# Performance work log

Measured on AMD Instinct MI355X. Metric: run time of the kernel, lower is better.

Reference implementation:

```python
import jax, jax.numpy as jnp
import numpy as np

N = 4096   # num_agents
F = 512    # feat_dim
P = 512    # phi_dim
A = 512    # aggr_dim
S = 6      # state_dim
H = 20     # MLP hidden width (hidden_layers=(20,20))


def _lstm(X, wih, whh, b):
    # torch.nn.LSTM single layer on an unbatched sequence X: [T, in] -> [T, hidden]
    pre = X @ wih + b  # [T, 4*hidden]
    Fh = whh.shape[0]
    def step(carry, p):
        h, c = carry
        g = p + h @ whh
        i, f, gg, o = jnp.split(g, 4, axis=-1)  # torch gate order: i, f, g, o
        c = jax.nn.sigmoid(f) * c + jax.nn.sigmoid(i) * jnp.tanh(gg)
        h = jax.nn.sigmoid(o) * jnp.tanh(c)
        return (h, c), h
    init = (jnp.zeros((Fh,), X.dtype), jnp.zeros((Fh,), X.dtype))
    _, hs = jax.lax.scan(step, init, pre)
    return hs


def setup_inputs():
    key = jax.random.key(0)
    ks = jax.random.split(key, 30)
    def rn(k, shape, s=0.05):
        return (jax.random.normal(k, shape) * s).astype(jnp.float32)
    x = jax.random.normal(ks[0], (N, F), dtype=jnp.float32)
    states = jax.random.normal(ks[1], (N, S), dtype=jnp.float32)
    # one comm link per agent (E == N, required by update()'s concat with x)
    src = jax.random.randint(ks[2], (N,), 0, N)
    dst = jnp.arange(N)
    inp = dict(x=x, states=states, src=src, dst=dst)
    inp["phi_w0"] = rn(ks[3], (4, F + S, H)); inp["phi_b0"] = rn(ks[4], (4, H))
    inp["phi_w1"] = rn(ks[5], (4, H, H));     inp["phi_b1"] = rn(ks[6], (4, H))
    inp["phi_w2"] = rn(ks[7], (4, H, P));     inp["phi_b2"] = rn(ks[8], (4, P))
    inp["tq_w"] = rn(ks[9], (4, P, A));  inp["tq_b"] = rn(ks[10], (4, A))
    inp["tk_w"] = rn(ks[11], (4, P, A)); inp["tk_b"] = rn(ks[12], (4, A))
    inp["tv_w"] = rn(ks[13], (4, P, A)); inp["tv_b"] = rn(ks[14], (4, A))
    inp["ts_w"] = rn(ks[15], (4, P, A)); inp["ts_b"] = rn(ks[16], (4, A))
    inp["wih0"] = rn(ks[17], (4, A + F, 4 * F)); inp["whh0"] = rn(ks[18], (4, F, 4 * F))
    inp["b0"] = rn(ks[19], (4, 4 * F))
    inp["wih1"] = rn(ks[20], (4, F, 4 * F)); inp["whh1"] = rn(ks[21], (4, F, 4 * F))
    inp["b1"] = rn(ks[22], (4, 4 * F))
    inp["cbf_w"] = rn(ks[23], (F, 1)); inp["cbf_b"] = rn(ks[24], (1,))
    return inp


def reference(x, states, src, dst, phi_w0, phi_b0, phi_w1, phi_b1, phi_w2, phi_b2,
              tq_w, tq_b, tk_w, tk_b, tv_w, tv_b, ts_w, ts_b,
              wih0, whh0, b0, wih1, whh1, b1, cbf_w, cbf_b):
    inv_sqrt_a = 1.0 / jnp.sqrt(jnp.float32(A))

    def gnn_layer(l, xin):
        # message: phi(concat(x_j, states_j - states_i))  (j = src, i = dst)
        msg = jnp.concatenate([xin[src], states[src] - states[dst]], axis=1)  # [E, F+S]
        h = jax.nn.relu(msg @ phi_w0[l] + phi_b0[l])
        h = jax.nn.relu(h @ phi_w1[l] + phi_b1[l])
        phi = h @ phi_w2[l] + phi_b2[l]  # [E, P]
        # aggregate: TransformerConv over message rows (E == N), heads=1
        q = phi @ tq_w[l] + tq_b[l]
        k = phi @ tk_w[l] + tk_b[l]
        v = phi @ tv_w[l] + tv_b[l]
        logits = jnp.sum(q[dst] * k[src], axis=-1) * inv_sqrt_a  # [E]
        m = jax.ops.segment_max(logits, dst, num_segments=N)
        e = jnp.exp(logits - m[dst])
        ssum = jax.ops.segment_sum(e, dst, num_segments=N)
        alpha = e / ssum[dst]
        aggr = jax.ops.segment_sum(alpha[:, None] * v[src], dst, num_segments=N)
        aggr = aggr + phi @ ts_w[l] + ts_b[l]  # root/skip connection
        # update: 2-layer LSTM over agents as an unbatched sequence
        gi = jnp.concatenate([aggr, xin], axis=1)  # [N, A+F]
        h0 = _lstm(gi, wih0[l], whh0[l], b0[l])
        h1 = _lstm(h0, wih1[l], whh1[l], b1[l])
        return h1

    xcur = gnn_layer(0, x)
    xcur = jax.nn.relu(xcur)
    xcur = gnn_layer(1, xcur)
    xcur = gnn_layer(2, xcur)      # feat_transformer layer 1
    xcur = jax.nn.relu(xcur)
    xcur = gnn_layer(3, xcur)      # feat_transformer layer 2
    hcbf = jax.nn.relu(xcur) @ cbf_w + cbf_b  # feat_2_CBF
    return xcur, hcbf
```

## Files before the change

kernel.cpp:

```cpp
#include <hip/hip_runtime.h>
#include <hip/hip_bf16.h>
#include <math.h>

#define NA   4096
#define FDIM 512
#define SDIM 6
#define HID  20
#define GDIM 2048
#define LWG  32

__device__ __forceinline__ float sigf(float x) { return 1.0f / (1.0f + __expf(-x)); }
__device__ __forceinline__ float tanh_fast(float x) {
    float e = __expf(2.0f * x);
    return 1.0f - 2.0f / (e + 1.0f);
}

__device__ __forceinline__ void atomicMaxF(float* addr, float v) {
    if (v >= 0.0f) atomicMax((int*)addr, __float_as_int(v));
    else           atomicMin((unsigned int*)addr, __float_as_uint(v));
}

__global__ void __launch_bounds__(256)
phi_fused(const float* __restrict__ xin, const float* __restrict__ states,
          const int* __restrict__ src, const int* __restrict__ dst,
          const float* __restrict__ w0, const float* __restrict__ b0,
          const float* __restrict__ w1, const float* __restrict__ b1,
          const float* __restrict__ w2, const float* __restrict__ b2,
          float* __restrict__ phi)
{
    int e = blockIdx.x, tid = threadIdx.x;
    __shared__ float msgv[FDIM + SDIM];
    __shared__ float red[240];
    __shared__ float hb1[HID];
    __shared__ float hb2[HID];
    int s = src[e], d = dst[e];
    for (int i = tid; i < FDIM; i += 256) msgv[i] = xin[(size_t)s * FDIM + i];
    if (tid < SDIM) msgv[FDIM + tid] = states[s * SDIM + tid] - states[d * SDIM + tid];
    __syncthreads();
    if (tid < 240) {
        int col = tid / 12, sg = tid % 12;
        int k0 = sg * 44, k1 = min(FDIM + SDIM, k0 + 44);
        float acc = 0.0f;
        for (int k = k0; k < k1; k++) acc += msgv[k] * w0[k * HID + col];
        red[tid] = acc;
    }
    __syncthreads();
    if (tid < HID) {
        float a = b0[tid];
#pragma unroll
        for (int q = 0; q < 12; q++) a += red[tid * 12 + q];
        hb1[tid] = fmaxf(a, 0.0f);
    }
    __syncthreads();
    if (tid < HID) {
        float a = b1[tid];
#pragma unroll
        for (int k = 0; k < HID; k++) a += hb1[k] * w1[k * HID + tid];
        hb2[tid] = fmaxf(a, 0.0f);
    }
    __syncthreads();
    for (int c = tid; c < FDIM; c += 256) {
        float a = b2[c];
#pragma unroll
        for (int k = 0; k < HID; k++) a += hb2[k] * w2[k * FDIM + c];
        phi[(size_t)e * FDIM + c] = a;
    }
}

struct Ptrs4 {
    const float* B[4];
    const float* bias[4];
    float* C[4];
};

__global__ void __launch_bounds__(256)
gemm128(const float* __restrict__ A1, int lda1,
        const float* __restrict__ A2, int lda2, int splitA,
        Ptrs4 p, int M, int N, int K)
{
    __shared__ float a_lds[16][132];
    __shared__ float b_lds[16][132];
    const float* __restrict__ B    = p.B[blockIdx.z];
    const float* __restrict__ bias = p.bias[blockIdx.z];
    float* __restrict__ C          = p.C[blockIdx.z];
    const int tid = threadIdx.x;
    const int m0 = blockIdx.y * 128, n0 = blockIdx.x * 128;
    const int ar = tid >> 2, ak4 = (tid & 3) * 4;
    const int br = tid >> 5, bc4 = (tid & 31) * 4;
    const int ty = tid >> 4, tx = tid & 15;
    float acc[8][8] = {};

    for (int kt = 0; kt < K; kt += 16) {
        int ak = kt + ak4;
        const float* abase;
        int acol;
        if (ak < splitA) { abase = A1; acol = ak;
            const float* r0 = abase + (size_t)(m0 + ar) * lda1 + acol;
            const float* r1 = abase + (size_t)(m0 + ar + 64) * lda1 + acol;
            float4 a0 = *(const float4*)r0;
            float4 a1 = *(const float4*)r1;
            a_lds[ak4 + 0][ar] = a0.x; a_lds[ak4 + 1][ar] = a0.y;
            a_lds[ak4 + 2][ar] = a0.z; a_lds[ak4 + 3][ar] = a0.w;
            a_lds[ak4 + 0][ar + 64] = a1.x; a_lds[ak4 + 1][ar + 64] = a1.y;
            a_lds[ak4 + 2][ar + 64] = a1.z; a_lds[ak4 + 3][ar + 64] = a1.w;
        } else {
            acol = ak - splitA;
            const float* r0 = A2 + (size_t)(m0 + ar) * lda2 + acol;
            const float* r1 = A2 + (size_t)(m0 + ar + 64) * lda2 + acol;
            float4 a0 = *(const float4*)r0;
            float4 a1 = *(const float4*)r1;
            a_lds[ak4 + 0][ar] = a0.x; a_lds[ak4 + 1][ar] = a0.y;
            a_lds[ak4 + 2][ar] = a0.z; a_lds[ak4 + 3][ar] = a0.w;
            a_lds[ak4 + 0][ar + 64] = a1.x; a_lds[ak4 + 1][ar + 64] = a1.y;
            a_lds[ak4 + 2][ar + 64] = a1.z; a_lds[ak4 + 3][ar + 64] = a1.w;
        }
        {
            float4 b0v = *(const float4*)(B + (size_t)(kt + br) * N + n0 + bc4);
            float4 b1v = *(const float4*)(B + (size_t)(kt + br + 8) * N + n0 + bc4);
            *(float4*)&b_lds[br][bc4] = b0v;
            *(float4*)&b_lds[br + 8][bc4] = b1v;
        }
        __syncthreads();
#pragma unroll
        for (int kk = 0; kk < 16; kk++) {
            float av[8], bv[8];
            *(float4*)&av[0] = *(const float4*)&a_lds[kk][ty * 4];
            *(float4*)&av[4] = *(const float4*)&a_lds[kk][64 + ty * 4];
            *(float4*)&bv[0] = *(const float4*)&b_lds[kk][tx * 4];
            *(float4*)&bv[4] = *(const float4*)&b_lds[kk][64 + tx * 4];
#pragma unroll
            for (int i = 0; i < 8; i++)
#pragma unroll
                for (int j = 0; j < 8; j++)
                    acc[i][j] += av[i] * bv[j];
        }
        __syncthreads();
    }

    float4 bb0 = *(const float4*)(bias + n0 + tx * 4);
    float4 bb1 = *(const float4*)(bias + n0 + 64 + tx * 4);
    const float bbs0[4] = { bb0.x, bb0.y, bb0.z, bb0.w };
    const float bbs1[4] = { bb1.x, bb1.y, bb1.z, bb1.w };
#pragma unroll
    for (int i = 0; i < 8; i++) {
        int row = m0 + ((i < 4) ? (ty * 4 + i) : (64 + ty * 4 + i - 4));
        float4 o0, o1;
        o0.x = acc[i][0] + bbs0[0]; o0.y = acc[i][1] + bbs0[1];
        o0.z = acc[i][2] + bbs0[2]; o0.w = acc[i][3] + bbs0[3];
        o1.x = acc[i][4] + bbs1[0]; o1.y = acc[i][5] + bbs1[1];
        o1.z = acc[i][6] + bbs1[2]; o1.w = acc[i][7] + bbs1[3];
        *(float4*)&C[(size_t)row * N + n0 + tx * 4] = o0;
        *(float4*)&C[(size_t)row * N + n0 + 64 + tx * 4] = o1;
    }
}

__global__ void att_init(float* __restrict__ m, float* __restrict__ ssum)
{
    int i = blockIdx.x * blockDim.x + threadIdx.x;
    if (i < NA) { m[i] = -INFINITY; ssum[i] = 0.0f; }
}

__global__ void att_logits(const float* __restrict__ q, const float* __restrict__ k,
                           const int* __restrict__ src, const int* __restrict__ dst,
                           float* __restrict__ logits, float* __restrict__ m)
{
    int e = blockIdx.x, tid = threadIdx.x;
    int s = src[e], d = dst[e];
    const float4* qr = (const float4*)(q + (size_t)d * FDIM);
    const float4* kr = (const float4*)(k + (size_t)s * FDIM);
    float acc = 0.0f;
    for (int i = tid; i < FDIM / 4; i += 64) {
        float4 a = qr[i], b = kr[i];
        acc += a.x * b.x + a.y * b.y + a.z * b.z + a.w * b.w;
    }
    for (int off = 32; off; off >>= 1) acc += __shfl_down(acc, off);
    if (tid == 0) {
        float v = acc * 0.04419417382415922f;
        logits[e] = v;
        atomicMaxF(&m[d], v);
    }
}

__global__ void att_expsum(const float* __restrict__ logits, const float* __restrict__ m,
                           const int* __restrict__ dst,
                           float* __restrict__ ebuf, float* __restrict__ ssum)
{
    int e = blockIdx.x * blockDim.x + threadIdx.x;
    if (e < NA) {
        float v = __expf(logits[e] - m[dst[e]]);
        ebuf[e] = v;
        atomicAdd(&ssum[dst[e]], v);
    }
}

__global__ void att_scatter(const float* __restrict__ v, const int* __restrict__ src,
                            const int* __restrict__ dst, const float* __restrict__ ebuf,
                            const float* __restrict__ ssum, float* __restrict__ aggr)
{
    int e = blockIdx.x, tid = threadIdx.x;
    int s = src[e], d = dst[e];
    float alpha = ebuf[e] / ssum[d];
    const float* vr = v + (size_t)s * FDIM;
    float* ar = aggr + (size_t)d * FDIM;
    for (int c = tid; c < FDIM; c += 256) atomicAdd(&ar[c], alpha * vr[c]);
}

__global__ void __launch_bounds__(512, 2)
lstm_pair(const float* __restrict__ pre0, const float* __restrict__ whh0,
          const float* __restrict__ wih1, const float* __restrict__ whh1,
          const float* __restrict__ b1,
          float* __restrict__ xout,
          unsigned long long* __restrict__ hfull,
          unsigned long long* __restrict__ hbuf1,
          unsigned int tag0, unsigned int tag1, int T)
{
    const int wg = blockIdx.x;
    const bool roleB = wg >= LWG;
    const int w = wg & (LWG - 1);
    const int tid = threadIdx.x;
    const int dl = tid & 15;
    const int gate = (tid >> 4) & 3;
    const int seg = tid >> 6;
    const int j = gate * 512 + w * 16 + dl;

    float wreg[128];
    if (!roleB) {
        const float* wc = whh0 + (size_t)(seg * 64) * GDIM + j;
#pragma unroll
        for (int kk = 0; kk < 64; kk++) wreg[kk] = wc[(size_t)kk * GDIM];
    } else {
        const float* wc = (seg < 4)
            ? (wih1 + (size_t)(seg * 128) * GDIM + j)
            : (whh1 + (size_t)((seg - 4) * 128) * GDIM + j);
#pragma unroll
        for (int kk = 0; kk < 128; kk++) wreg[kk] = wc[(size_t)kk * GDIM];
    }

    __shared__ float h_lds[1024];
    __shared__ float red[512];
    __shared__ float gbuf[64];
    float c = 0.0f;
    float extra = 0.0f;
    if (tid < 64) extra = roleB ? b1[j] : pre0[j];
    if (!roleB) h_lds[tid] = 0.0f;
    else        h_lds[512 + tid] = 0.0f;
    __syncthreads();

    if (!roleB) {
        for (int t = 0; t < T; t++) {
            const float* hseg = h_lds + seg * 64;
            float a0 = 0, a1 = 0, a2 = 0, a3 = 0;
#pragma unroll
            for (int kk = 0; kk < 64; kk += 4) {
                float4 hv = *(const float4*)(hseg + kk);
                a0 += wreg[kk + 0] * hv.x;
                a1 += wreg[kk + 1] * hv.y;
                a2 += wreg[kk + 2] * hv.z;
                a3 += wreg[kk + 3] * hv.w;
            }
            red[tid] = (a0 + a1) + (a2 + a3);
            __syncthreads();
            if (tid < 64) {
                float tot = extra;
#pragma unroll
                for (int s = 0; s < 8; s++) tot += red[tid + 64 * s];
                gbuf[tid] = tot;
                if (t + 1 < T) extra = pre0[(size_t)(t + 1) * GDIM + j];
            }
            __syncthreads();
            if (tid < 16) {
                float ii = gbuf[tid], ff = gbuf[16 + tid], gg = gbuf[32 + tid], oo = gbuf[48 + tid];
                c = sigf(ff) * c + sigf(ii) * tanh_fast(gg);
                float h = sigf(oo) * tanh_fast(c);
                unsigned long long word =
                    ((unsigned long long)(tag0 + (unsigned)t + 1u) << 32) |
                    (unsigned long long)__float_as_uint(h);
                __hip_atomic_store(&hfull[(size_t)t * 512 + w * 16 + tid], word,
                                   __ATOMIC_RELAXED, __HIP_MEMORY_SCOPE_AGENT);
            }
            if (t + 1 < T) {
                unsigned long long want = tag0 + (unsigned)t + 1u;
                const unsigned long long* p = &hfull[(size_t)t * 512 + tid];
                unsigned long long v = __hip_atomic_load(p, __ATOMIC_RELAXED, __HIP_MEMORY_SCOPE_AGENT);
                while ((v >> 32) != want)
                    v = __hip_atomic_load(p, __ATOMIC_RELAXED, __HIP_MEMORY_SCOPE_AGENT);
                h_lds[tid] = __uint_as_float((unsigned)v);
                __syncthreads();
            }
        }
    } else {
        for (int t = 0; t < T; t++) {
            {
                unsigned long long want = tag0 + (unsigned)t + 1u;
                const unsigned long long* p = &hfull[(size_t)t * 512 + tid];
                unsigned long long v = __hip_atomic_load(p, __ATOMIC_RELAXED, __HIP_MEMORY_SCOPE_AGENT);
                while ((v >> 32) != want)
                    v = __hip_atomic_load(p, __ATOMIC_RELAXED, __HIP_MEMORY_SCOPE_AGENT);
                h_lds[tid] = __uint_as_float((unsigned)v);
            }
            __syncthreads();
            const float* hseg = h_lds + seg * 128;
            float a0 = 0, a1 = 0, a2 = 0, a3 = 0;
#pragma unroll
            for (int kk = 0; kk < 128; kk += 4) {
                float4 hv = *(const float4*)(hseg + kk);
                a0 += wreg[kk + 0] * hv.x;
                a1 += wreg[kk + 1] * hv.y;
                a2 += wreg[kk + 2] * hv.z;
                a3 += wreg[kk + 3] * hv.w;
            }
            red[tid] = (a0 + a1) + (a2 + a3);
            __syncthreads();
            if (tid < 64) {
                float tot = extra;
#pragma unroll
                for (int s = 0; s < 8; s++) tot += red[tid + 64 * s];
                gbuf[tid] = tot;
            }
            __syncthreads();
            if (tid < 16) {
                float ii = gbuf[tid], ff = gbuf[16 + tid], gg = gbuf[32 + tid], oo = gbuf[48 + tid];
                c = sigf(ff) * c + sigf(ii) * tanh_fast(gg);
                float h = sigf(oo) * tanh_fast(c);
                xout[(size_t)t * 512 + w * 16 + tid] = h;
                unsigned long long word =
                    ((unsigned long long)(tag1 + (unsigned)t + 1u) << 32) |
                    (unsigned long long)__float_as_uint(h);
                __hip_atomic_store(&hbuf1[(t & 1) * 512 + w * 16 + tid], word,
                                   __ATOMIC_RELAXED, __HIP_MEMORY_SCOPE_AGENT);
            }
            if (t + 1 < T) {
                unsigned long long want = tag1 + (unsigned)t + 1u;
                const unsigned long long* p = &hbuf1[(t & 1) * 512 + tid];
                unsigned long long v = __hip_atomic_load(p, __ATOMIC_RELAXED, __HIP_MEMORY_SCOPE_AGENT);
                while ((v >> 32) != want)
                    v = __hip_atomic_load(p, __ATOMIC_RELAXED, __HIP_MEMORY_SCOPE_AGENT);
                h_lds[512 + tid] = __uint_as_float((unsigned)v);
                __syncthreads();
            }
        }
    }
}

__global__ void relu_ip(float* __restrict__ x, int n)
{
    int i = blockIdx.x * blockDim.x + threadIdx.x;
    if (i < n) x[i] = fmaxf(x[i], 0.0f);
}

__global__ void cbf_head(const float* __restrict__ xc, const float* __restrict__ w,
                         const float* __restrict__ b, float* __restrict__ out)
{
    int i = blockIdx.x, tid = threadIdx.x;
    const float* xr = xc + (size_t)i * FDIM;
    float acc = 0.0f;
    for (int d = tid; d < FDIM; d += 64) acc += fmaxf(xr[d], 0.0f) * w[d];
    for (int off = 32; off; off >>= 1) acc += __shfl_down(acc, off);
    if (tid == 0) out[i] = acc + b[0];
}

__global__ void zero_u64(unsigned long long* __restrict__ p, int n)
{
    int i = blockIdx.x * blockDim.x + threadIdx.x;
    int stride = gridDim.x * blockDim.x;
    for (; i < n; i += stride) p[i] = 0ull;
}

extern "C" void kernel_launch(void* const* d_in, const int* in_sizes, int n_in,
                              void* d_out, int out_size, void* d_ws, size_t ws_size,
                              hipStream_t stream)
{
    const float* x      = (const float*)d_in[0];
    const float* states = (const float*)d_in[1];
    const int*   src    = (const int*)d_in[2];
    const int*   dst    = (const int*)d_in[3];
    const float* phi_w0 = (const float*)d_in[4];
    const float* phi_b0 = (const float*)d_in[5];
    const float* phi_w1 = (const float*)d_in[6];
    const float* phi_b1 = (const float*)d_in[7];
    const float* phi_w2 = (const float*)d_in[8];
    const float* phi_b2 = (const float*)d_in[9];
    const float* tq_w = (const float*)d_in[10]; const float* tq_b = (const float*)d_in[11];
    const float* tk_w = (const float*)d_in[12]; const float* tk_b = (const float*)d_in[13];
    const float* tv_w = (const float*)d_in[14]; const float* tv_b = (const float*)d_in[15];
    const float* ts_w = (const float*)d_in[16]; const float* ts_b = (const float*)d_in[17];
    const float* wih0 = (const float*)d_in[18]; const float* whh0 = (const float*)d_in[19];
    const float* b0   = (const float*)d_in[20];
    const float* wih1 = (const float*)d_in[21]; const float* whh1 = (const float*)d_in[22];
    const float* b1   = (const float*)d_in[23];
    const float* cbf_w = (const float*)d_in[24]; const float* cbf_b = (const float*)d_in[25];

    float* ws = (float*)d_ws;
    size_t off = 0;
    auto alloc = [&](size_t n) { float* p = ws + off; off += n; return p; };
    float* xA     = alloc((size_t)NA * FDIM);
    float* xB     = alloc((size_t)NA * FDIM);
    float* phi    = alloc((size_t)NA * FDIM);
    float* qb     = alloc((size_t)NA * FDIM);
    float* kb     = alloc((size_t)NA * FDIM);
    float* vb     = alloc((size_t)NA * FDIM);
    float* aggr   = alloc((size_t)NA * FDIM);
    float* pre    = alloc((size_t)NA * GDIM);
    float* logits = alloc(NA);
    float* mb     = alloc(NA);
    float* ssum   = alloc(NA);
    float* ebuf   = alloc(NA);
    const int HFULL_WORDS = NA * 512;
    unsigned long long* hfull = (unsigned long long*)alloc((size_t)2 * (HFULL_WORDS + 1024));
    unsigned long long* hbuf1 = hfull + HFULL_WORDS;

    float* out_x   = (float*)d_out;
    float* out_cbf = out_x + (size_t)NA * FDIM;

    zero_u64<<<2048, 256, 0, stream>>>(hfull, HFULL_WORDS + 1024);

    const float* xin = x;
    for (int l = 0; l < 4; l++) {
        float* xout = (l == 3) ? out_x : ((l & 1) ? xB : xA);

        phi_fused<<<NA, 256, 0, stream>>>(xin, states, src, dst,
            phi_w0 + (size_t)l * 518 * HID, phi_b0 + l * HID,
            phi_w1 + (size_t)l * HID * HID, phi_b1 + l * HID,
            phi_w2 + (size_t)l * HID * FDIM, phi_b2 + l * FDIM, phi);

        {
            Ptrs4 p;
            p.B[0] = tq_w + (size_t)l * FDIM * FDIM; p.bias[0] = tq_b + l * FDIM; p.C[0] = qb;
            p.B[1] = tk_w + (size_t)l * FDIM * FDIM; p.bias[1] = tk_b + l * FDIM; p.C[1] = kb;
            p.B[2] = tv_w + (size_t)l * FDIM * FDIM; p.bias[2] = tv_b + l * FDIM; p.C[2] = vb;
            p.B[3] = ts_w + (size_t)l * FDIM * FDIM; p.bias[3] = ts_b + l * FDIM; p.C[3] = aggr;
            gemm128<<<dim3(FDIM / 128, NA / 128, 4), 256, 0, stream>>>(
                phi, FDIM, phi, FDIM, FDIM, p, NA, FDIM, FDIM);
        }

        att_init<<<NA / 256, 256, 0, stream>>>(mb, ssum);
        att_logits<<<NA, 64, 0, stream>>>(qb, kb, src, dst, logits, mb);
        att_expsum<<<NA / 256, 256, 0, stream>>>(logits, mb, dst, ebuf, ssum);
        att_scatter<<<NA, 256, 0, stream>>>(vb, src, dst, ebuf, ssum, aggr);

        {
            Ptrs4 p;
            p.B[0] = wih0 + (size_t)l * 1024 * GDIM; p.bias[0] = b0 + (size_t)l * GDIM; p.C[0] = pre;
            p.B[1] = p.B[0]; p.bias[1] = p.bias[0]; p.C[1] = pre;
            p.B[2] = p.B[0]; p.bias[2] = p.bias[0]; p.C[2] = pre;
            p.B[3] = p.B[0]; p.bias[3] = p.bias[0]; p.C[3] = pre;
            gemm128<<<dim3(GDIM / 128, NA / 128, 1), 256, 0, stream>>>(
                aggr, FDIM, xin, FDIM, FDIM, p, NA, GDIM, 1024);
        }

        lstm_pair<<<2 * LWG, 512, 0, stream>>>(pre,
            whh0 + (size_t)l * FDIM * GDIM,
            wih1 + (size_t)l * FDIM * GDIM,
            whh1 + (size_t)l * FDIM * GDIM,
            b1 + (size_t)l * GDIM,
            xout, hfull, hbuf1,
            (unsigned)(2 * l) * NA, (unsigned)(2 * l + 1) * NA, NA);

        if (l == 0 || l == 2)
            relu_ip<<<(NA * FDIM + 255) / 256, 256, 0, stream>>>(xout, NA * FDIM);
        xin = xout;
    }

    cbf_head<<<NA, 64, 0, stream>>>(out_x, cbf_w, cbf_b, out_cbf);
}
```

Baseline: 38.41 ms.

## Restructure LSTM recurrence to reduce gates within a wavefront via shuffles

```diff
diff --git a/kernel.cpp b/kernel.cpp
--- a/kernel.cpp
+++ b/kernel.cpp
@@ -8,6 +8,8 @@
 #define HID  20
 #define GDIM 2048
 #define LWG  32
+
+typedef unsigned long long u64;
 
 __device__ __forceinline__ float sigf(float x) { return 1.0f / (1.0f + __expf(-x)); }
 __device__ __forceinline__ float tanh_fast(float x) {
@@ -92,11 +94,9 @@
 
     for (int kt = 0; kt < K; kt += 16) {
         int ak = kt + ak4;
-        const float* abase;
-        int acol;
-        if (ak < splitA) { abase = A1; acol = ak;
-            const float* r0 = abase + (size_t)(m0 + ar) * lda1 + acol;
-            const float* r1 = abase + (size_t)(m0 + ar + 64) * lda1 + acol;
+        if (ak < splitA) {
+            const float* r0 = A1 + (size_t)(m0 + ar) * lda1 + ak;
+            const float* r1 = A1 + (size_t)(m0 + ar + 64) * lda1 + ak;
             float4 a0 = *(const float4*)r0;
             float4 a1 = *(const float4*)r1;
             a_lds[ak4 + 0][ar] = a0.x; a_lds[ak4 + 1][ar] = a0.y;
@@ -104,7 +104,7 @@
             a_lds[ak4 + 0][ar + 64] = a1.x; a_lds[ak4 + 1][ar + 64] = a1.y;
             a_lds[ak4 + 2][ar + 64] = a1.z; a_lds[ak4 + 3][ar + 64] = a1.w;
         } else {
-            acol = ak - splitA;
+            int acol = ak - splitA;
             const float* r0 = A2 + (size_t)(m0 + ar) * lda2 + acol;
             const float* r1 = A2 + (size_t)(m0 + ar + 64) * lda2 + acol;
             float4 a0 = *(const float4*)r0;
@@ -210,18 +210,25 @@
           const float* __restrict__ wih1, const float* __restrict__ whh1,
           const float* __restrict__ b1,
           float* __restrict__ xout,
-          unsigned long long* __restrict__ hfull,
-          unsigned long long* __restrict__ hbuf1,
+          u64* __restrict__ hfull,
+          u64* __restrict__ hbuf1,
           unsigned int tag0, unsigned int tag1, int T)
 {
     const int wg = blockIdx.x;
     const bool roleB = wg >= LWG;
     const int w = wg & (LWG - 1);
     const int tid = threadIdx.x;
-    const int dl = tid & 15;
-    const int gate = (tid >> 4) & 3;
-    const int seg = tid >> 6;
-    const int j = gate * 512 + w * 16 + dl;
+    const int lane = tid & 63;
+    const int wv = tid >> 6;
+    const int c = lane & 7;
+    const int seg = lane >> 3;
+    const int gate = c >> 1;
+    const int dimoff = c & 1;
+    const int hd = w * 16 + wv * 2 + dimoff;
+    const int j = gate * 512 + hd;
+
+    __shared__ float buf[2][1088];
+    for (int i = tid; i < 1088; i += 512) { buf[0][i] = 0.0f; buf[1][i] = 0.0f; }
 
     float wreg[128];
     if (!roleB) {
@@ -229,114 +236,119 @@
 #pragma unroll
         for (int kk = 0; kk < 64; kk++) wreg[kk] = wc[(size_t)kk * GDIM];
     } else {
-        const float* wc = (seg < 4)
-            ? (wih1 + (size_t)(seg * 128) * GDIM + j)
-            : (whh1 + (size_t)((seg - 4) * 128) * GDIM + j);
-#pragma unroll
-        for (int kk = 0; kk < 128; kk++) wreg[kk] = wc[(size_t)kk * GDIM];
-    }
-
-    __shared__ float h_lds[1024];
-    __shared__ float red[512];
-    __shared__ float gbuf[64];
-    float c = 0.0f;
-    float extra = 0.0f;
-    if (tid < 64) extra = roleB ? b1[j] : pre0[j];
-    if (!roleB) h_lds[tid] = 0.0f;
-    else        h_lds[512 + tid] = 0.0f;
+#pragma unroll
+        for (int kk = 0; kk < 128; kk++) {
+            int k = seg * 128 + kk;
+            wreg[kk] = (k < 512) ? wih1[(size_t)k * GDIM + j]
+                                 : whh1[(size_t)(k - 512) * GDIM + j];
+        }
+    }
     __syncthreads();
 
+    const int gbase = (lane & 56) | dimoff;
+
     if (!roleB) {
+        float cst = 0.0f;
+        float pre_nxt = pre0[j];
+        int p = 0;
         for (int t = 0; t < T; t++) {
-            const float* hseg = h_lds + seg * 64;
+            const float* hb = &buf[p][seg * 68];
             float a0 = 0, a1 = 0, a2 = 0, a3 = 0;
 #pragma unroll
             for (int kk = 0; kk < 64; kk += 4) {
-                float4 hv = *(const float4*)(hseg + kk);
+                float4 hv = *(const float4*)(hb + kk);
                 a0 += wreg[kk + 0] * hv.x;
                 a1 += wreg[kk + 1] * hv.y;
                 a2 += wreg[kk + 2] * hv.z;
                 a3 += wreg[kk + 3] * hv.w;
             }
-            red[tid] = (a0 + a1) + (a2 + a3);
-            __syncthreads();
-            if (tid < 64) {
-                float tot = extra;
-#pragma unroll
-                for (int s = 0; s < 8; s++) tot += red[tid + 64 * s];
-                gbuf[tid] = tot;
-                if (t + 1 < T) extra = pre0[(size_t)(t + 1) * GDIM + j];
-            }
-            __syncthreads();
-            if (tid < 16) {
-                float ii = gbuf[tid], ff = gbuf[16 + tid], gg = gbuf[32 + tid], oo = gbuf[48 + tid];
-                c = sigf(ff) * c + sigf(ii) * tanh_fast(gg);
-                float h = sigf(oo) * tanh_fast(c);
-                unsigned long long word =
-                    ((unsigned long long)(tag0 + (unsigned)t + 1u) << 32) |
-                    (unsigned long long)__float_as_uint(h);
-                __hip_atomic_store(&hfull[(size_t)t * 512 + w * 16 + tid], word,
+            float tot = (a0 + a1) + (a2 + a3);
+            tot += __shfl_xor(tot, 8);
+            tot += __shfl_xor(tot, 16);
+            tot += __shfl_xor(tot, 32);
+            tot += pre_nxt;
+            if (t + 1 < T) pre_nxt = pre0[(size_t)(t + 1) * GDIM + j];
+            float nl = (gate == 2) ? tanh_fast(tot) : sigf(tot);
+            float ff = __shfl(nl, gbase | 2);
+            float gg = __shfl(nl, gbase | 4);
+            float oo = __shfl(nl, gbase | 6);
+            if (c < 2) {
+                cst = ff * cst + nl * gg;
+                float h = oo * tanh_fast(cst);
+                u64 word = ((u64)(tag0 + (unsigned)t + 1u) << 32) |
+                           (u64)__float_as_uint(h);
+                __hip_atomic_store(&hfull[(size_t)t * 512 + hd], word,
                                    __ATOMIC_RELAXED, __HIP_MEMORY_SCOPE_AGENT);
             }
             if (t + 1 < T) {
-                unsigned long long want = tag0 + (unsigned)t + 1u;
-                const unsigned long long* p = &hfull[(size_t)t * 512 + tid];
-                unsigned long long v = __hip_atomic_load(p, __ATOMIC_RELAXED, __HIP_MEMORY_SCOPE_AGENT);
+                u64 want = tag0 + (unsigned)t + 1u;
+                const u64* pp = &hfull[(size_t)t * 512 + tid];
+                u64 v = __hip_atomic_load(pp, __ATOMIC_RELAXED, __HIP_MEMORY_SCOPE_AGENT);
                 while ((v >> 32) != want)
-                    v = __hip_atomic_load(p, __ATOMIC_RELAXED, __HIP_MEMORY_SCOPE_AGENT);
-                h_lds[tid] = __uint_as_float((unsigned)v);
+                    v = __hip_atomic_load(pp, __ATOMIC_RELAXED, __HIP_MEMORY_SCOPE_AGENT);
+                buf[p ^ 1][(tid >> 6) * 68 + (tid & 63)] = __uint_as_float((unsigned)v);
                 __syncthreads();
+                p ^= 1;
             }
         }
     } else {
+        float cst = 0.0f;
+        float bias = b1[j];
+        int p = 0;
         for (int t = 0; t < T; t++) {
             {
-                unsigned long long want = tag0 + (unsigned)t + 1u;
-                const unsigned long long* p = &hfull[(size_t)t * 512 + tid];
-                unsigned long long v = __hip_atomic_load(p, __ATOMIC_RELAXED, __HIP_MEMORY_SCOPE_AGENT);
+                u64 want = tag0 + (unsigned)t + 1u;
+                const u64* pp = &hfull[(size_t)t * 512 + tid];
+                u64 v = __hip_atomic_load(pp, __ATOMIC_RELAXED, __HIP_MEMORY_SCOPE_AGENT);
                 while ((v >> 32) != want)
-                    v = __hip_atomic_load(p, __ATOMIC_RELAXED, __HIP_MEMORY_SCOPE_AGENT);
-                h_lds[tid] = __uint_as_float((unsigned)v);
+                    v = __hip_atomic_load(pp, __ATOMIC_RELAXED, __HIP_MEMORY_SCOPE_AGENT);
+                buf[p][(tid >> 6) * 68 + (tid & 63)] = __uint_as_float((unsigned)v);
             }
             __syncthreads();
-            const float* hseg = h_lds + seg * 128;
+            const float* hb = &buf[p][seg * 136];
             float a0 = 0, a1 = 0, a2 = 0, a3 = 0;
 #pragma unroll
-            for (int kk = 0; kk < 128; kk += 4) {
-                float4 hv = *(const float4*)(hseg + kk);
+            for (int kk = 0; kk < 64; kk += 4) {
+                float4 hv = *(const float4*)(hb + kk);
                 a0 += wreg[kk + 0] * hv.x;
                 a1 += wreg[kk + 1] * hv.y;
                 a2 += wreg[kk + 2] * hv.z;
                 a3 += wreg[kk + 3] * hv.w;
             }
-            red[tid] = (a0 + a1) + (a2 + a3);
-            __syncthreads();
-            if (tid < 64) {
-                float tot = extra;
-#pragma unroll
-                for (int s = 0; s < 8; s++) tot += red[tid + 64 * s];
-                gbuf[tid] = tot;
-            }
-            __syncthreads();
-            if (tid < 16) {
-                float ii = gbuf[tid], ff = gbuf[16 + tid], gg = gbuf[32 + tid], oo = gbuf[48 + tid];
-                c = sigf(ff) * c + sigf(ii) * tanh_fast(gg);
-                float h = sigf(oo) * tanh_fast(c);
-                xout[(size_t)t * 512 + w * 16 + tid] = h;
-                unsigned long long word =
-                    ((unsigned long long)(tag1 + (unsigned)t + 1u) << 32) |
-                    (unsigned long long)__float_as_uint(h);
-                __hip_atomic_store(&hbuf1[(t & 1) * 512 + w * 16 + tid], word,
+#pragma unroll
+            for (int kk = 0; kk < 64; kk += 4) {
+                float4 hv = *(const float4*)(hb + 68 + kk);
+                a0 += wreg[64 + kk + 0] * hv.x;
+                a1 += wreg[64 + kk + 1] * hv.y;
+                a2 += wreg[64 + kk + 2] * hv.z;
+                a3 += wreg[64 + kk + 3] * hv.w;
+            }
+            float tot = (a0 + a1) + (a2 + a3);
+            tot += __shfl_xor(tot, 8);
+            tot += __shfl_xor(tot, 16);
+            tot += __shfl_xor(tot, 32);
+            tot += bias;
+            float nl = (gate == 2) ? tanh_fast(tot) : sigf(tot);
+            float ff = __shfl(nl, gbase | 2);
+            float gg = __shfl(nl, gbase | 4);
+            float oo = __shfl(nl, gbase | 6);
+            if (c < 2) {
+                cst = ff * cst + nl * gg;
+                float h = oo * tanh_fast(cst);
+                xout[(size_t)t * 512 + hd] = h;
+                u64 word = ((u64)(tag1 + (unsigned)t + 1u) << 32) |
+                           (u64)__float_as_uint(h);
+                __hip_atomic_store(&hbuf1[(t & 1) * 512 + hd], word,
                                    __ATOMIC_RELAXED, __HIP_MEMORY_SCOPE_AGENT);
             }
             if (t + 1 < T) {
-                unsigned long long want = tag1 + (unsigned)t + 1u;
-                const unsigned long long* p = &hbuf1[(t & 1) * 512 + tid];
-                unsigned long long v = __hip_atomic_load(p, __ATOMIC_RELAXED, __HIP_MEMORY_SCOPE_AGENT);
+                u64 want = tag1 + (unsigned)t + 1u;
+                const u64* pp = &hbuf1[(t & 1) * 512 + tid];
+                u64 v = __hip_atomic_load(pp, __ATOMIC_RELAXED, __HIP_MEMORY_SCOPE_AGENT);
                 while ((v >> 32) != want)
-                    v = __hip_atomic_load(p, __ATOMIC_RELAXED, __HIP_MEMORY_SCOPE_AGENT);
-                h_lds[512 + tid] = __uint_as_float((unsigned)v);
-                __syncthreads();
+                    v = __hip_atomic_load(pp, __ATOMIC_RELAXED, __HIP_MEMORY_SCOPE_AGENT);
+                buf[p ^ 1][(8 + (tid >> 6)) * 68 + (tid & 63)] = __uint_as_float((unsigned)v);
+                p ^= 1;
             }
         }
     }
@@ -359,7 +371,7 @@
     if (tid == 0) out[i] = acc + b[0];
 }
 
-__global__ void zero_u64(unsigned long long* __restrict__ p, int n)
+__global__ void zero_u64(u64* __restrict__ p, int n)
 {
     int i = blockIdx.x * blockDim.x + threadIdx.x;
     int stride = gridDim.x * blockDim.x;
@@ -406,8 +418,8 @@
     float* ssum   = alloc(NA);
     float* ebuf   = alloc(NA);
     const int HFULL_WORDS = NA * 512;
-    unsigned long long* hfull = (unsigned long long*)alloc((size_t)2 * (HFULL_WORDS + 1024));
-    unsigned long long* hbuf1 = hfull + HFULL_WORDS;
+    u64* hfull = (u64*)alloc((size_t)2 * (HFULL_WORDS + 1024));
+    u64* hbuf1 = hfull + HFULL_WORDS;
 
     float* out_x   = (float*)d_out;
     float* out_cbf = out_x + (size_t)NA * FDIM;
```

Measured after the change: 49.83 ms. 29.7% more time.
